# Performance work log

Hardware: AMD Instinct MI355X
Metric: run time of the kernel (lower is better)

Reference implementation:

```python
import jax, jax.numpy as jnp
import numpy as np

BATCH = 256
SIZE = 512      # must be a power of two for the bitonic network
K = 16          # top-k
STEEPNESS = 10.0  # cauchy distribution scale (module default)


def _bitonic_layers(n):
    """Static index pairs of the bitonic sorting network (ascending).
    Returns (lefts, rights), each int32 [n_layers, n//2]. After a compare-swap,
    the soft-min goes to `left` and the soft-max goes to `right`."""
    lefts, rights = [], []
    k = 2
    while k <= n:
        j = k // 2
        while j >= 1:
            l_idx, r_idx = [], []
            for i in range(n):
                l = i ^ j
                if l > i:
                    if (i & k) == 0:   # ascending block: min at i
                        l_idx.append(i); r_idx.append(l)
                    else:              # descending block: min at l
                        l_idx.append(l); r_idx.append(i)
            lefts.append(l_idx); rights.append(r_idx)
            j //= 2
        k *= 2
    return np.asarray(lefts, np.int32), np.asarray(rights, np.int32)


def setup_inputs() -> dict:
    key = jax.random.key(0)
    vectors = jax.random.normal(key, (BATCH, SIZE), dtype=jnp.float32)
    return {"vectors": vectors}


def reference(vectors):
    b, n = vectors.shape
    lefts_np, rights_np = _bitonic_layers(n)
    lefts = jnp.asarray(lefts_np)
    rights = jnp.asarray(rights_np)
    # soft permutation matrix: X[b, i, j] = P(input j ends at sorted pos i)
    X0 = jnp.broadcast_to(jnp.eye(n, dtype=vectors.dtype)[None], (b, n, n))

    def step(carry, lr):
        x, X = carry
        l, r = lr                      # [n//2] index pairs for this layer
        a = x[:, l]                    # [b, n//2]
        c = x[:, r]
        # cauchy CDF of steepness*(c - a): prob that no swap is needed
        alpha = jnp.arctan((c - a) * STEEPNESS) / jnp.pi + 0.5
        x = x.at[:, l].set(alpha * a + (1.0 - alpha) * c)
        x = x.at[:, r].set(alpha * c + (1.0 - alpha) * a)
        Xl = X[:, l, :]                # [b, n//2, n]
        Xr = X[:, r, :]
        al = alpha[..., None]
        X = X.at[:, l, :].set(al * Xl + (1.0 - al) * Xr)
        X = X.at[:, r, :].set(al * Xr + (1.0 - al) * Xl)
        return (x, X), None

    (_, X), _ = jax.lax.scan(step, (vectors, X0), (lefts, rights))
    # ascending sort -> last K rows correspond to the K largest elements;
    # flip so row 0 = largest. Output: [batch, K, n] soft top-k distribution.
    return jnp.flip(X[:, n - K:, :], axis=1)
```

## Files before the change

kernel.cpp:

```cpp
#include <hip/hip_runtime.h>
#include <math.h>

#define N 512
#define BATCH 256
#define KTOP 16
#define NLAYERS 45
#define NPAIRS 256

template<int CTRL>
__device__ __forceinline__ float dpp_xor(float x) {
    return __int_as_float(
        __builtin_amdgcn_mov_dpp(__float_as_int(x), CTRL, 0xF, 0xF, true));
}

__device__ __forceinline__ float fast_alpha(float t) {
    const float at  = __builtin_fabsf(t);
    const bool inv  = at > 1.0f;
    const float z   = inv ? __builtin_amdgcn_rcpf(at) : at;
    const float s   = z * z;
    float p = -0.0117212f;
    p = __builtin_fmaf(p, s,  0.05265332f);
    p = __builtin_fmaf(p, s, -0.11643287f);
    p = __builtin_fmaf(p, s,  0.19354346f);
    p = __builtin_fmaf(p, s, -0.33262347f);
    p = __builtin_fmaf(p, s,  0.99997726f);
    float r = z * p;
    r = inv ? (1.5707963267948966f - r) : r;
    r = (t < 0.0f) ? -r : r;
    return __builtin_fmaf(r, 0.3183098861837907f, 0.5f);
}

__global__ __launch_bounds__(512, 2)
void difftopk_kernel(const float* __restrict__ x_in, float* __restrict__ out) {
    __shared__ float xs[2][N];
    __shared__ __align__(16) float As[NLAYERS][NPAIRS];

    const int b    = blockIdx.x;
    const int e    = threadIdx.x;
    const int lane = e & 63;

    float o = x_in[(size_t)b * N + e];

    int t = 0, par = 0;
    #pragma unroll
    for (int s = 1; s <= 9; ++s) {
        const int k  = 1 << s;
        const bool kb = (e & k) == 0;
        #pragma unroll
        for (int lg = s - 1; lg >= 0; --lg, ++t) {
            const int j = 1 << lg;
            float p;
            if (lg >= 6) {
                xs[par][e] = o;
                __syncthreads();
                p = xs[par][e ^ j];
                par ^= 1;
            } else if (lg == 0) {
                p = dpp_xor<0xB1>(o);
            } else if (lg == 1) {
                p = dpp_xor<0x4E>(o);
            } else if (lg == 3) {
                p = dpp_xor<0x128>(o);
            } else {
                p = __shfl_xor(o, j, 64);
            }
            const bool jb = (e & j) == 0;
            const float d = (kb == jb) ? (p - o) : (o - p);
            const float alpha = fast_alpha(d * 10.0f);
            o = __builtin_fmaf(alpha, o - p, p);
            if (jb) {
                const int ord = ((e >> (lg + 1)) << lg) | (e & (j - 1));
                As[t][ord] = alpha;
            }
        }
    }
    __syncthreads();

    const int wave  = e >> 6;
    const int lane8 = lane << 3;
    const int r0 = N - 1 - wave;
    const int r1 = N - 1 - (wave + 8);

    float v0[8], v1[8];
    #pragma unroll
    for (int m = 0; m < 8; ++m) {
        v0[m] = (lane8 + m == r0) ? 1.0f : 0.0f;
        v1[m] = (lane8 + m == r1) ? 1.0f : 0.0f;
    }

    #pragma unroll
    for (int s = 9; s >= 1; --s) {
        const int base = (s * (s - 1)) >> 1;
        #pragma unroll
        for (int lg = 0; lg < s; ++lg) {
            const int tt = base + (s - 1 - lg);
            if (lg >= 3) {
                const int j    = 1 << lg;
                const int ordb = ((lane8 >> (lg + 1)) << lg) | (lane8 & (j - 1));
                const float4 a0 = *(const float4*)&As[tt][ordb];
                const float4 a1 = *(const float4*)&As[tt][ordb + 4];
                const float al[8] = {a0.x, a0.y, a0.z, a0.w, a1.x, a1.y, a1.z, a1.w};
                #pragma unroll
                for (int m = 0; m < 8; ++m) {
                    float p0, p1;
                    if (lg == 3)      { p0 = dpp_xor<0xB1>(v0[m]);  p1 = dpp_xor<0xB1>(v1[m]);  }
                    else if (lg == 4) { p0 = dpp_xor<0x4E>(v0[m]);  p1 = dpp_xor<0x4E>(v1[m]);  }
                    else if (lg == 6) { p0 = dpp_xor<0x128>(v0[m]); p1 = dpp_xor<0x128>(v1[m]); }
                    else              { p0 = __shfl_xor(v0[m], j >> 3, 64);
                                        p1 = __shfl_xor(v1[m], j >> 3, 64); }
                    v0[m] = __builtin_fmaf(al[m], v0[m] - p0, p0);
                    v1[m] = __builtin_fmaf(al[m], v1[m] - p1, p1);
                }
            } else {
                const float4 a = *(const float4*)&As[tt][lane << 2];
                const float aa[4] = {a.x, a.y, a.z, a.w};
                float n0[8], n1[8];
                if (lg == 2) {
                    #pragma unroll
                    for (int m = 0; m < 8; ++m) {
                        const float al = aa[m & 3];
                        n0[m] = __builtin_fmaf(al, v0[m] - v0[m ^ 4], v0[m ^ 4]);
                        n1[m] = __builtin_fmaf(al, v1[m] - v1[m ^ 4], v1[m ^ 4]);
                    }
                } else if (lg == 1) {
                    #pragma unroll
                    for (int m = 0; m < 8; ++m) {
                        const float al = aa[((m >> 2) << 1) | (m & 1)];
                        n0[m] = __builtin_fmaf(al, v0[m] - v0[m ^ 2], v0[m ^ 2]);
                        n1[m] = __builtin_fmaf(al, v1[m] - v1[m ^ 2], v1[m ^ 2]);
                    }
                } else {
                    #pragma unroll
                    for (int m = 0; m < 8; ++m) {
                        const float al = aa[m >> 1];
                        n0[m] = __builtin_fmaf(al, v0[m] - v0[m ^ 1], v0[m ^ 1]);
                        n1[m] = __builtin_fmaf(al, v1[m] - v1[m ^ 1], v1[m ^ 1]);
                    }
                }
                #pragma unroll
                for (int m = 0; m < 8; ++m) { v0[m] = n0[m]; v1[m] = n1[m]; }
            }
        }
    }

    float4* dst0 = (float4*)(out + ((size_t)b * KTOP + wave) * N + lane8);
    dst0[0] = make_float4(v0[0], v0[1], v0[2], v0[3]);
    dst0[1] = make_float4(v0[4], v0[5], v0[6], v0[7]);
    float4* dst1 = (float4*)(out + ((size_t)b * KTOP + wave + 8) * N + lane8);
    dst1[0] = make_float4(v1[0], v1[1], v1[2], v1[3]);
    dst1[1] = make_float4(v1[4], v1[5], v1[6], v1[7]);
}

extern "C" void kernel_launch(void* const* d_in, const int* in_sizes, int n_in,
                              void* d_out, int out_size, void* d_ws, size_t ws_size,
                              hipStream_t stream) {
    const float* x = (const float*)d_in[0];
    float* out = (float*)d_out;
    difftopk_kernel<<<dim3(BATCH), dim3(512), 0, stream>>>(x, out);
}
```

Before: 65.71 us.

## Use 1024-thread blocks so each wave back-propagates one output row

Blocks grow to 1024 threads. The first 512 run the forward bitonic network while the extra 512 only match its 7 barriers. In the backward phase each of the 16 waves carries a single output row instead of two, which halves the per-thread register arrays. The lg<3 in-register butterflies are rewritten to update pairs in place without temporary copies. The cost is half the threads idling during the forward phase and one block per CU instead of two, which may reduce latency hiding.

```diff
diff --git a/kernel.cpp b/kernel.cpp
--- a/kernel.cpp
+++ b/kernel.cpp
@@ -30,63 +30,65 @@
     return __builtin_fmaf(r, 0.3183098861837907f, 0.5f);
 }
 
-__global__ __launch_bounds__(512, 2)
+__global__ __launch_bounds__(1024, 1)
 void difftopk_kernel(const float* __restrict__ x_in, float* __restrict__ out) {
     __shared__ float xs[2][N];
     __shared__ __align__(16) float As[NLAYERS][NPAIRS];
 
     const int b    = blockIdx.x;
-    const int e    = threadIdx.x;
-    const int lane = e & 63;
+    const int tid  = threadIdx.x;
+    const int lane = tid & 63;
 
-    float o = x_in[(size_t)b * N + e];
+    if (tid < N) {
+        const int e = tid;
+        float o = x_in[(size_t)b * N + e];
 
-    int t = 0, par = 0;
-    #pragma unroll
-    for (int s = 1; s <= 9; ++s) {
-        const int k  = 1 << s;
-        const bool kb = (e & k) == 0;
+        int t = 0, par = 0;
         #pragma unroll
-        for (int lg = s - 1; lg >= 0; --lg, ++t) {
-            const int j = 1 << lg;
-            float p;
-            if (lg >= 6) {
-                xs[par][e] = o;
-                __syncthreads();
-                p = xs[par][e ^ j];
-                par ^= 1;
-            } else if (lg == 0) {
-                p = dpp_xor<0xB1>(o);
-            } else if (lg == 1) {
-                p = dpp_xor<0x4E>(o);
-            } else if (lg == 3) {
-                p = dpp_xor<0x128>(o);
-            } else {
-                p = __shfl_xor(o, j, 64);
-            }
-            const bool jb = (e & j) == 0;
-            const float d = (kb == jb) ? (p - o) : (o - p);
-            const float alpha = fast_alpha(d * 10.0f);
-            o = __builtin_fmaf(alpha, o - p, p);
-            if (jb) {
-                const int ord = ((e >> (lg + 1)) << lg) | (e & (j - 1));
-                As[t][ord] = alpha;
+        for (int s = 1; s <= 9; ++s) {
+            const int k  = 1 << s;
+            const bool kb = (e & k) == 0;
+            #pragma unroll
+            for (int lg = s - 1; lg >= 0; --lg, ++t) {
+                const int j = 1 << lg;
+                float p;
+                if (lg >= 6) {
+                    xs[par][e] = o;
+                    __syncthreads();
+                    p = xs[par][e ^ j];
+                    par ^= 1;
+                } else if (lg == 0) {
+                    p = dpp_xor<0xB1>(o);
+                } else if (lg == 1) {
+                    p = dpp_xor<0x4E>(o);
+                } else if (lg == 3) {
+                    p = dpp_xor<0x128>(o);
+                } else {
+                    p = __shfl_xor(o, j, 64);
+                }
+                const bool jb = (e & j) == 0;
+                const float d = (kb == jb) ? (p - o) : (o - p);
+                const float alpha = fast_alpha(d * 10.0f);
+                o = __builtin_fmaf(alpha, o - p, p);
+                if (jb) {
+                    const int ord = ((e >> (lg + 1)) << lg) | (e & (j - 1));
+                    As[t][ord] = alpha;
+                }
             }
         }
+        __syncthreads();
+    } else {
+        #pragma unroll 1
+        for (int i = 0; i < 7; ++i) __syncthreads();
     }
-    __syncthreads();
 
-    const int wave  = e >> 6;
+    const int wave  = tid >> 6;
     const int lane8 = lane << 3;
-    const int r0 = N - 1 - wave;
-    const int r1 = N - 1 - (wave + 8);
+    const int r     = N - 1 - wave;
 
-    float v0[8], v1[8];
+    float v[8];
     #pragma unroll
-    for (int m = 0; m < 8; ++m) {
-        v0[m] = (lane8 + m == r0) ? 1.0f : 0.0f;
-        v1[m] = (lane8 + m == r1) ? 1.0f : 0.0f;
-    }
+    for (int m = 0; m < 8; ++m) v[m] = (lane8 + m == r) ? 1.0f : 0.0f;
 
     #pragma unroll
     for (int s = 9; s >= 1; --s) {
@@ -102,53 +104,47 @@
                 const float al[8] = {a0.x, a0.y, a0.z, a0.w, a1.x, a1.y, a1.z, a1.w};
                 #pragma unroll
                 for (int m = 0; m < 8; ++m) {
-                    float p0, p1;
-                    if (lg == 3)      { p0 = dpp_xor<0xB1>(v0[m]);  p1 = dpp_xor<0xB1>(v1[m]);  }
-                    else if (lg == 4) { p0 = dpp_xor<0x4E>(v0[m]);  p1 = dpp_xor<0x4E>(v1[m]);  }
-                    else if (lg == 6) { p0 = dpp_xor<0x128>(v0[m]); p1 = dpp_xor<0x128>(v1[m]); }
-                    else              { p0 = __shfl_xor(v0[m], j >> 3, 64);
-                                        p1 = __shfl_xor(v1[m], j >> 3, 64); }
-                    v0[m] = __builtin_fmaf(al[m], v0[m] - p0, p0);
-                    v1[m] = __builtin_fmaf(al[m], v1[m] - p1, p1);
+                    float p;
+                    if (lg == 3)      p = dpp_xor<0xB1>(v[m]);
+                    else if (lg == 4) p = dpp_xor<0x4E>(v[m]);
+                    else if (lg == 6) p = dpp_xor<0x128>(v[m]);
+                    else              p = __shfl_xor(v[m], j >> 3, 64);
+                    v[m] = __builtin_fmaf(al[m], v[m] - p, p);
                 }
             } else {
                 const float4 a = *(const float4*)&As[tt][lane << 2];
                 const float aa[4] = {a.x, a.y, a.z, a.w};
-                float n0[8], n1[8];
                 if (lg == 2) {
                     #pragma unroll
-                    for (int m = 0; m < 8; ++m) {
-                        const float al = aa[m & 3];
-                        n0[m] = __builtin_fmaf(al, v0[m] - v0[m ^ 4], v0[m ^ 4]);
-                        n1[m] = __builtin_fmaf(al, v1[m] - v1[m ^ 4], v1[m ^ 4]);
+                    for (int i = 0; i < 4; ++i) {
+                        const float x0 = v[i], x1 = v[i + 4], d = x0 - x1;
+                        v[i]     = __builtin_fmaf(aa[i],  d, x1);
+                        v[i + 4] = __builtin_fmaf(aa[i], -d, x0);
                     }
                 } else if (lg == 1) {
                     #pragma unroll
-                    for (int m = 0; m < 8; ++m) {
-                        const float al = aa[((m >> 2) << 1) | (m & 1)];
-                        n0[m] = __builtin_fmaf(al, v0[m] - v0[m ^ 2], v0[m ^ 2]);
-                        n1[m] = __builtin_fmaf(al, v1[m] - v1[m ^ 2], v1[m ^ 2]);
+                    for (int i = 0; i < 4; ++i) {
+                        const int lo = (((i >> 1) << 2) | (i & 1));
+                        const float x0 = v[lo], x1 = v[lo + 2], d = x0 - x1;
+                        v[lo]     = __builtin_fmaf(aa[i],  d, x1);
+                        v[lo + 2] = __builtin_fmaf(aa[i], -d, x0);
                     }
                 } else {
                     #pragma unroll
-                    for (int m = 0; m < 8; ++m) {
-                        const float al = aa[m >> 1];
-                        n0[m] = __builtin_fmaf(al, v0[m] - v0[m ^ 1], v0[m ^ 1]);
-                        n1[m] = __builtin_fmaf(al, v1[m] - v1[m ^ 1], v1[m ^ 1]);
+                    for (int i = 0; i < 4; ++i) {
+                        const int lo = i << 1;
+                        const float x0 = v[lo], x1 = v[lo + 1], d = x0 - x1;
+                        v[lo]     = __builtin_fmaf(aa[i],  d, x1);
+                        v[lo + 1] = __builtin_fmaf(aa[i], -d, x0);
                     }
                 }
-                #pragma unroll
-                for (int m = 0; m < 8; ++m) { v0[m] = n0[m]; v1[m] = n1[m]; }
             }
         }
     }
 
-    float4* dst0 = (float4*)(out + ((size_t)b * KTOP + wave) * N + lane8);
-    dst0[0] = make_float4(v0[0], v0[1], v0[2], v0[3]);
-    dst0[1] = make_float4(v0[4], v0[5], v0[6], v0[7]);
-    float4* dst1 = (float4*)(out + ((size_t)b * KTOP + wave + 8) * N + lane8);
-    dst1[0] = make_float4(v1[0], v1[1], v1[2], v1[3]);
-    dst1[1] = make_float4(v1[4], v1[5], v1[6], v1[7]);
+    float4* dst = (float4*)(out + ((size_t)b * KTOP + wave) * N + lane8);
+    dst[0] = make_float4(v[0], v[1], v[2], v[3]);
+    dst[1] = make_float4(v[4], v[5], v[6], v[7]);
 }
 
 extern "C" void kernel_launch(void* const* d_in, const int* in_sizes, int n_in,
@@ -156,5 +152,5 @@
                               hipStream_t stream) {
     const float* x = (const float*)d_in[0];
     float* out = (float*)d_out;
-    difftopk_kernel<<<dim3(BATCH), dim3(512), 0, stream>>>(x, out);
+    difftopk_kernel<<<dim3(BATCH), dim3(1024), 0, stream>>>(x, out);
 }
```

After: 65.70 us. No clear change (-0.0%).
